# Kernel optimization log

Measured on AMD Instinct MI355X. Metric: run time of the kernel, lower is better.

Reference implementation:

```python
import jax, jax.numpy as jnp
import numpy as np
import math

H, P = 8, 4  # n_heads, num_points


def _interp1d(values, idx):
    # values: (B,H,Lk,D); idx: (B,H,Lq,P) float positions in [0, Lk-1]
    B, h, Lk, D = values.shape
    Lq, p = idx.shape[2], idx.shape[3]
    idx0 = jnp.clip(jnp.floor(idx), 0, Lk - 1).astype(jnp.int32)
    idx1 = jnp.clip(idx0 + 1, 0, Lk - 1)
    w1 = (idx - idx0.astype(idx.dtype))[..., None]          # (B,H,Lq,P,1)
    g0 = jnp.take_along_axis(values, idx0.reshape(B, h, Lq * p)[..., None], axis=2)
    g1 = jnp.take_along_axis(values, idx1.reshape(B, h, Lq * p)[..., None], axis=2)
    g0 = g0.reshape(B, h, Lq, p, D)
    g1 = g1.reshape(B, h, Lq, p, D)
    return (1.0 - w1) * g0 + w1 * g1                         # (B,H,Lq,P,D)


def setup_inputs() -> dict:
    key = jax.random.key(0)
    ks = jax.random.split(key, 8)
    B, L, dm = 4, 4096, 512
    s = 0.02
    return {
        'q_in': jax.random.normal(ks[0], (B, L, dm), jnp.float32),
        'kv_in': jax.random.normal(ks[1], (B, L, dm), jnp.float32),
        'Wq': jax.random.normal(ks[2], (dm, dm), jnp.float32) * s,
        'bq': jnp.zeros((dm,), jnp.float32),
        'Wk': jax.random.normal(ks[3], (dm, dm), jnp.float32) * s,
        'bk': jnp.zeros((dm,), jnp.float32),
        'Wv': jax.random.normal(ks[4], (dm, dm), jnp.float32) * s,
        'bv': jnp.zeros((dm,), jnp.float32),
        'Woff': jax.random.normal(ks[5], (H * P, dm), jnp.float32) * s,
        'boff': jnp.zeros((H * P,), jnp.float32),
        'Wa': jax.random.normal(ks[6], (H * P, dm), jnp.float32) * s,
        'ba': jnp.zeros((H * P,), jnp.float32),
        'Wo': jax.random.normal(ks[7], (dm, dm), jnp.float32) * s,
        'bo': jnp.zeros((dm,), jnp.float32),
    }


def reference(q_in, kv_in, Wq, bq, Wk, bk, Wv, bv, Woff, boff, Wa, ba, Wo, bo):
    B, Lq, dm = q_in.shape
    Lk = kv_in.shape[1]
    D = dm // H
    q = (q_in @ Wq.T + bq).reshape(B, Lq, H, D).transpose(0, 2, 1, 3)   # (B,H,Lq,D)
    k = (kv_in @ Wk.T + bk).reshape(B, Lk, H, D).transpose(0, 2, 1, 3)  # (B,H,Lk,D)
    v = (kv_in @ Wv.T + bv).reshape(B, Lk, H, D).transpose(0, 2, 1, 3)
    offsets = (q_in @ Woff.T + boff).reshape(B, Lq, H, P).transpose(0, 2, 1, 3)  # (B,H,Lq,P)
    logits = (q_in @ Wa.T + ba).reshape(B, Lq, H, P).transpose(0, 2, 1, 3)
    if Lq == Lk:
        base = jnp.arange(Lq, dtype=q_in.dtype).reshape(1, 1, Lq, 1)
    else:
        base = jnp.linspace(0.0, Lk - 1, Lq, dtype=q_in.dtype).reshape(1, 1, Lq, 1)
    idx = jnp.clip(base + offsets, 0.0, float(Lk - 1))
    k_s = _interp1d(k, idx)  # (B,H,Lq,P,D)
    v_s = _interp1d(v, idx)
    dot = jnp.einsum('bhld,bhlpd->bhlp', q, k_s) / math.sqrt(D)
    w = jax.nn.softmax(dot + logits, axis=-1)               # (B,H,Lq,P)
    out = jnp.einsum('bhlp,bhlpd->bhld', w, v_s)            # (B,H,Lq,D)
    out = out.transpose(0, 2, 1, 3).reshape(B, Lq, dm)
    return out @ Wo.T + bo
```

## Files before the change

kernel.cpp:

```cpp
#include <hip/hip_runtime.h>
#include <hip/hip_bf16.h>
#include <math.h>

#define NH 8
#define NP 4
#define DD 64
#define DM 512

typedef unsigned short u16;
typedef unsigned int u32;

using frag_ab = __attribute__((ext_vector_type(8))) short;
using f32x4   = __attribute__((ext_vector_type(4))) float;

__device__ __forceinline__ u16 f2b(float f) {
    u32 u = __float_as_uint(f);
    u32 r = (u + 0x7FFFu + ((u >> 16) & 1u)) >> 16;
    return (u16)r;
}
__device__ __forceinline__ u32 pk2(float x, float y) {
    float2 t; t.x = x; t.y = y;
    __hip_bfloat162 h = __float22bfloat162_rn(t);
    return *(u32*)&h;
}

#define GLOBAL_AS __attribute__((address_space(1)))
#define LDS_AS    __attribute__((address_space(3)))
__device__ __forceinline__ void async_copy16(void* lds, const void* g) {
    __builtin_amdgcn_global_load_lds((const GLOBAL_AS u32*)g, (LDS_AS u32*)lds, 16, 0, 0);
}

#define VMW4_BARRIER() do {                                   \
    asm volatile("s_waitcnt vmcnt(4)" ::: "memory");          \
    __builtin_amdgcn_s_barrier();                             \
    __builtin_amdgcn_sched_barrier(0); } while (0)
#define VMW2_BARRIER() do {                                   \
    asm volatile("s_waitcnt vmcnt(2)" ::: "memory");          \
    __builtin_amdgcn_s_barrier();                             \
    __builtin_amdgcn_sched_barrier(0); } while (0)
#define VMW0_BARRIER() do {                                   \
    asm volatile("s_waitcnt vmcnt(0)" ::: "memory");          \
    __builtin_amdgcn_s_barrier();                             \
    __builtin_amdgcn_sched_barrier(0); } while (0)

__device__ __forceinline__ void compute_phase(
    const u16* __restrict__ sa, const u16* __restrict__ sb,
    int wrow, int wcol, int lr, int kgs, f32x4 (&acc)[4][4])
{
    frag_ab af[4], bfr[4];
#pragma unroll
    for (int i = 0; i < 4; ++i)
        af[i] = *(const frag_ab*)&sa[(wrow + i * 16 + lr) * 32 + kgs];
#pragma unroll
    for (int j = 0; j < 4; ++j)
        bfr[j] = *(const frag_ab*)&sb[(wcol + j * 16 + lr) * 32 + kgs];
    asm volatile("s_waitcnt lgkmcnt(0)" ::: "memory");
    __builtin_amdgcn_s_barrier();
    __builtin_amdgcn_sched_barrier(0);
#pragma unroll
    for (int i = 0; i < 4; ++i)
#pragma unroll
        for (int j = 0; j < 4; ++j)
            acc[i][j] = __builtin_amdgcn_mfma_f32_16x16x32_bf16(
                af[i], bfr[j], acc[i][j], 0, 0, 0);
}

__global__ __launch_bounds__(256) void proj_gemm(
    const u16* __restrict__ q_bf, const u16* __restrict__ kv_bf,
    const u16* __restrict__ Wcat1, const u16* __restrict__ Wcat2,
    const float* __restrict__ bcat1, const float* __restrict__ bcat2,
    u16* __restrict__ q_ws, float* __restrict__ offlog,
    u16* __restrict__ kv_ws)
{
    constexpr int BM = 128, BK = 32;
    __shared__ u16 sA0[BM * BK], sA1[BM * BK];
    __shared__ u16 sB0[BM * BK], sB1[BM * BK];

    const int tid  = threadIdx.x;
    const int wave = tid >> 6;
    const int lane = tid & 63;
    const int m0 = blockIdx.x * BM;
    const bool is_q = blockIdx.y < 5;
    const int n0 = (is_q ? blockIdx.y : blockIdx.y - 5) * BM;
    const int Ncur = is_q ? 576 : 1024;
    const u16* __restrict__ A    = is_q ? q_bf : kv_bf;
    const u16* __restrict__ Wt   = is_q ? Wcat1 : Wcat2;
    const float* __restrict__ bias = is_q ? bcat1 : bcat2;

    const int wrow = 64 * (wave >> 1);
    const int wcol = 64 * (wave & 1);

    f32x4 acc[4][4] = {};
    const int lr = lane & 15;
    const int kg = lane >> 4;
    const int kgs = ((kg ^ ((lr >> 1) & 3)) << 3);
    const int sgo = (((lane & 3) ^ ((lane >> 3) & 3)) << 3);

    float bv4[4];
#pragma unroll
    for (int j = 0; j < 4; ++j)
        bv4[j] = bias[n0 + wcol + j * 16 + lr];

    const int cA = wave * 64 + lane;
    const size_t arow0 = (size_t)(m0 + (cA >> 2)) * DM + sgo;
    const int cA2 = (4 + wave) * 64 + lane;
    const size_t arow1 = (size_t)(m0 + (cA2 >> 2)) * DM + sgo;
    const size_t brow0 = (size_t)(n0 + (cA >> 2)) * DM + sgo;
    const size_t brow1 = (size_t)(n0 + (cA2 >> 2)) * DM + sgo;
    const int ldsA0 = wave * 512, ldsA1 = (4 + wave) * 512;

    auto stage = [&](u16* sa, u16* sb, int k0) {
        async_copy16(&sa[ldsA0], A + arow0 + k0);
        async_copy16(&sa[ldsA1], A + arow1 + k0);
        async_copy16(&sb[ldsA0], Wt + brow0 + k0);
        async_copy16(&sb[ldsA1], Wt + brow1 + k0);
    };

    stage(sA0, sB0, 0);

    for (int ktt = 0; ktt < 8; ++ktt) {
        stage(sA1, sB1, (2 * ktt + 1) << 5);
        VMW4_BARRIER();
        compute_phase(sA0, sB0, wrow, wcol, lr, kgs, acc);
        if (ktt < 7) {
            stage(sA0, sB0, (2 * ktt + 2) << 5);
            VMW4_BARRIER();
        } else {
            VMW0_BARRIER();
        }
        compute_phase(sA1, sB1, wrow, wcol, lr, kgs, acc);
    }

    const int crow0 = (lane >> 4) * 4;
#pragma unroll
    for (int i = 0; i < 4; ++i) {
#pragma unroll
        for (int j = 0; j < 4; ++j) {
            const int colbase = n0 + wcol + j * 16;
            if (colbase >= Ncur) continue;
            const int col = colbase + lr;
            const float bv = bv4[j];
#pragma unroll
            for (int r = 0; r < 4; ++r) {
                const int row = m0 + wrow + i * 16 + crow0 + r;
                const float val = acc[i][j][r] + bv;
                if (!is_q)
                    kv_ws[(size_t)row * 1024 + col] = f2b(val);
                else if (colbase < 512)
                    q_ws[(size_t)row * 512 + col] = f2b(val);
                else
                    offlog[(size_t)row * 64 + (col - 512)] = val;
            }
        }
    }
}

__device__ __forceinline__ void compute_phase8(
    const u16* __restrict__ sa, const u16* __restrict__ sb,
    int wrow, int wcol, int lr, int kgs, f32x4 (&acc)[4][2])
{
    frag_ab af[4], bfr[2];
#pragma unroll
    for (int i = 0; i < 4; ++i)
        af[i] = *(const frag_ab*)&sa[(wrow + i * 16 + lr) * 32 + kgs];
#pragma unroll
    for (int j = 0; j < 2; ++j)
        bfr[j] = *(const frag_ab*)&sb[(wcol + j * 16 + lr) * 32 + kgs];
    asm volatile("s_waitcnt lgkmcnt(0)" ::: "memory");
    __builtin_amdgcn_s_barrier();
    __builtin_amdgcn_sched_barrier(0);
#pragma unroll
    for (int i = 0; i < 4; ++i)
#pragma unroll
        for (int j = 0; j < 2; ++j)
            acc[i][j] = __builtin_amdgcn_mfma_f32_16x16x32_bf16(
                af[i], bfr[j], acc[i][j], 0, 0, 0);
}

__global__ __launch_bounds__(512) void out_gemm(
    const u16* __restrict__ A, const u16* __restrict__ Wt,
    const float* __restrict__ bias, float* __restrict__ C)
{
    constexpr int BM = 128, BK = 32;
    __shared__ u16 sA0[BM * BK], sA1[BM * BK];
    __shared__ u16 sB0[BM * BK], sB1[BM * BK];

    const int tid  = threadIdx.x;
    const int wave = tid >> 6;
    const int lane = tid & 63;
    const int m0 = blockIdx.x * BM;
    const int n0 = blockIdx.y * BM;

    const int wrow = 64 * (wave >> 2);
    const int wcol = 32 * (wave & 3);

    f32x4 acc[4][2] = {};
    const int lr = lane & 15;
    const int kg = lane >> 4;
    const int kgs = ((kg ^ ((lr >> 1) & 3)) << 3);
    const int sgo = (((tid & 3) ^ ((tid >> 3) & 3)) << 3);

    float bv2[2];
#pragma unroll
    for (int j = 0; j < 2; ++j)
        bv2[j] = bias[n0 + wcol + j * 16 + lr];

    const size_t arow = (size_t)(m0 + (tid >> 2)) * DM + sgo;
    const size_t brow = (size_t)(n0 + (tid >> 2)) * DM + sgo;
    const int ldsoff = tid * 8;

    auto stage = [&](u16* sa, u16* sb, int k0) {
        async_copy16(&sa[ldsoff], A + arow + k0);
        async_copy16(&sb[ldsoff], Wt + brow + k0);
    };

    stage(sA0, sB0, 0);

    for (int ktt = 0; ktt < 8; ++ktt) {
        stage(sA1, sB1, (2 * ktt + 1) << 5);
        VMW2_BARRIER();
        compute_phase8(sA0, sB0, wrow, wcol, lr, kgs, acc);
        if (ktt < 7) {
            stage(sA0, sB0, (2 * ktt + 2) << 5);
            VMW2_BARRIER();
        } else {
            VMW0_BARRIER();
        }
        compute_phase8(sA1, sB1, wrow, wcol, lr, kgs, acc);
    }

    const int crow0 = kg * 4;
#pragma unroll
    for (int i = 0; i < 4; ++i) {
#pragma unroll
        for (int j = 0; j < 2; ++j) {
            const int col = n0 + wcol + j * 16 + lr;
            const float bv = bv2[j];
#pragma unroll
            for (int r = 0; r < 4; ++r) {
                const int row = m0 + wrow + i * 16 + crow0 + r;
                C[(size_t)row * 512 + col] = acc[i][j][r] + bv;
            }
        }
    }
}

__global__ __launch_bounds__(256) void prep_weights(
    const float* __restrict__ Wq, const float* __restrict__ Woff,
    const float* __restrict__ Wa, const float* __restrict__ Wk,
    const float* __restrict__ Wv, const float* __restrict__ Wo,
    const float* __restrict__ bq, const float* __restrict__ boff,
    const float* __restrict__ ba, const float* __restrict__ bk,
    const float* __restrict__ bv,
    const float* __restrict__ q_in, const float* __restrict__ kv_in,
    u16* __restrict__ Wcat1, u16* __restrict__ Wcat2, u16* __restrict__ Wob,
    float* __restrict__ bcat1, float* __restrict__ bcat2,
    u16* __restrict__ q_bf, u16* __restrict__ kv_bf, int n8)
{
    const int W4  = 65536;
    const int W4s = 4096;
    const int WEND = 4 * W4 + 2 * W4s;
    const int BEND = WEND + 2048;
    int tid = blockIdx.x * 256 + threadIdx.x;
    if (tid < WEND) {
        const float* src; u16* dst; int off;
        int t = tid;
        if (t < W4)                    { src = Wq;    dst = Wcat1;           off = t; }
        else if ((t -= W4) < W4s)      { src = Woff;  dst = Wcat1 + 262144;  off = t; }
        else if ((t -= W4s) < W4s)     { src = Wa;    dst = Wcat1 + 278528;  off = t; }
        else if ((t -= W4s) < W4)      { src = Wk;    dst = Wcat2;           off = t; }
        else if ((t -= W4) < W4)       { src = Wv;    dst = Wcat2 + 262144;  off = t; }
        else                           { src = Wo;    dst = Wob;             off = t - W4; }
        float4 v = ((const float4*)src)[off];
        ushort4 o;
        o.x = f2b(v.x); o.y = f2b(v.y); o.z = f2b(v.z); o.w = f2b(v.w);
        ((ushort4*)dst)[off] = o;
    } else if (tid < BEND) {
        int j = tid - WEND;
        if (j < 576) {
            bcat1[j] = (j < 512) ? bq[j] : (j < 544 ? boff[j - 512] : ba[j - 544]);
        } else if (j < 1600) {
            int j2 = j - 576;
            bcat2[j2] = (j2 < 512) ? bk[j2] : bv[j2 - 512];
        }
    } else {
        int t = tid - BEND;
        if (t < 2 * n8) {
            const float* src; u16* dst; int off;
            if (t < n8) { src = q_in;  dst = q_bf;  off = t; }
            else        { src = kv_in; dst = kv_bf; off = t - n8; }
            float4 a = ((const float4*)src)[off * 2];
            float4 b = ((const float4*)src)[off * 2 + 1];
            uint4 w;
            w.x = pk2(a.x, a.y); w.y = pk2(a.z, a.w);
            w.z = pk2(b.x, b.y); w.w = pk2(b.z, b.w);
            ((uint4*)dst)[off] = w;
        }
    }
}

#define WAVE_SYNC() do {                                      \
    asm volatile("s_waitcnt lgkmcnt(0)" ::: "memory");        \
    __builtin_amdgcn_sched_barrier(0); } while (0)

__global__ __launch_bounds__(256) void deform_attn_band(
    const u16* __restrict__ q, const u16* __restrict__ kv,
    const float* __restrict__ offlog, u16* __restrict__ out, int B, int L)
{
    __shared__ u16  sVt[4][64 * 40];
    __shared__ float sS[4][16 * 36];
    __shared__ float sW[4][16 * 36];

    const int wave = threadIdx.x >> 6;
    const int lane = threadIdx.x & 63;
    const int gw = blockIdx.x * 4 + wave;
    const int nlb = L >> 4;
    const int lblk = gw % nlb;
    const int bh = gw / nlb;
    const int h = bh % NH;
    const int b = bh / NH;
    const int l0 = lblk << 4;

    u16*  __restrict__ vt = sVt[wave];
    float* __restrict__ Ss = sS[wave];
    float* __restrict__ Ws = sW[wave];

    const size_t brow = (size_t)b * L;
    const int headoff = h * DD;

    const int l_loc = lane >> 2, p = lane & 3;
    const size_t obase = (brow + l0 + l_loc) * 64 + h * 4 + p;
    const float offv  = offlog[obase];
    const float logit = offlog[obase + 32];

    const int fr = lane & 15, kg = lane >> 4;

    const u16* qrow = q + (brow + l0 + fr) * DM + headoff;
    frag_ab qf0 = *(const frag_ab*)(qrow + kg * 8);
    frag_ab qf1 = *(const frag_ab*)(qrow + kg * 8 + 32);

    frag_ab kf[2][2];
#pragma unroll
    for (int jf = 0; jf < 2; ++jf) {
        int rr = l0 - 8 + jf * 16 + fr;
        rr = min(max(rr, 0), L - 1);
        const u16* krow = kv + (brow + rr) * 1024 + headoff;
        kf[jf][0] = *(const frag_ab*)(krow + kg * 8);
        kf[jf][1] = *(const frag_ab*)(krow + kg * 8 + 32);
    }

    const int vr = lane & 31, vd0 = (lane >> 5) * 32;
    int vrr = min(max(l0 - 8 + vr, 0), L - 1);
    const u16* vrow = kv + (brow + vrr) * 1024 + 512 + headoff + vd0;
    frag_ab vl[4];
#pragma unroll
    for (int i = 0; i < 4; ++i)
        vl[i] = *(const frag_ab*)(vrow + i * 8);

    f32x4 accS[2] = {};
#pragma unroll
    for (int jf = 0; jf < 2; ++jf) {
        accS[jf] = __builtin_amdgcn_mfma_f32_16x16x32_bf16(qf0, kf[jf][0], accS[jf], 0, 0, 0);
        accS[jf] = __builtin_amdgcn_mfma_f32_16x16x32_bf16(qf1, kf[jf][1], accS[jf], 0, 0, 0);
    }

#pragma unroll
    for (int i = 0; i < 4; ++i)
#pragma unroll
        for (int j = 0; j < 8; ++j)
            vt[(vd0 + i * 8 + j) * 40 + vr] = (u16)vl[i][j];

#pragma unroll
    for (int jf = 0; jf < 2; ++jf)
#pragma unroll
        for (int r = 0; r < 4; ++r)
            Ss[(kg * 4 + r) * 36 + jf * 16 + fr] = accS[jf][r];

#pragma unroll
    for (int i = 0; i < 9; ++i)
        Ws[lane + 64 * i] = 0.f;

    WAVE_SYNC();

    float pos = fminf(fmaxf((float)(l0 + l_loc) + offv, 0.f), (float)(L - 1));
    float ff = floorf(pos);
    int i0 = (int)ff;
    float fw = pos - ff;
    int c0 = i0 - (l0 - 8);
    c0 = min(max(c0, 0), 30);
    float S0 = Ss[l_loc * 36 + c0];
    float S1 = Ss[l_loc * 36 + c0 + 1];
    float t = (S0 + fw * (S1 - S0)) * 0.125f + logit;
    float m1 = fmaxf(t, __shfl_xor(t, 1));
    float mx = fmaxf(m1, __shfl_xor(m1, 2));
    float e = __expf(t - mx);
    float s1 = e + __shfl_xor(e, 1);
    float ssum = s1 + __shfl_xor(s1, 2);
    float wgt = e * __builtin_amdgcn_rcpf(ssum);
    atomicAdd(&Ws[l_loc * 36 + c0], (1.f - fw) * wgt);
    atomicAdd(&Ws[l_loc * 36 + c0 + 1], fw * wgt);

    WAVE_SYNC();

    float4 w0 = *(const float4*)&Ws[fr * 36 + kg * 8];
    float4 w1 = *(const float4*)&Ws[fr * 36 + kg * 8 + 4];
    frag_ab wf;
    wf[0] = (short)f2b(w0.x); wf[1] = (short)f2b(w0.y);
    wf[2] = (short)f2b(w0.z); wf[3] = (short)f2b(w0.w);
    wf[4] = (short)f2b(w1.x); wf[5] = (short)f2b(w1.y);
    wf[6] = (short)f2b(w1.z); wf[7] = (short)f2b(w1.w);

#pragma unroll
    for (int md = 0; md < 4; ++md) {
        frag_ab af = *(const frag_ab*)&vt[(md * 16 + fr) * 40 + kg * 8];
        f32x4 o = {};
        o = __builtin_amdgcn_mfma_f32_16x16x32_bf16(af, wf, o, 0, 0, 0);
        ushort4 pk;
        pk.x = f2b(o[0]); pk.y = f2b(o[1]); pk.z = f2b(o[2]); pk.w = f2b(o[3]);
        *(ushort4*)&out[(brow + l0 + fr) * DM + headoff + md * 16 + kg * 4] = pk;
    }
}

extern "C" void kernel_launch(void* const* d_in, const int* in_sizes, int n_in,
                              void* d_out, int out_size, void* d_ws, size_t ws_size,
                              hipStream_t stream) {
    const float* q_in  = (const float*)d_in[0];
    const float* kv_in = (const float*)d_in[1];
    const float* Wq = (const float*)d_in[2];  const float* bq = (const float*)d_in[3];
    const float* Wk = (const float*)d_in[4];  const float* bk = (const float*)d_in[5];
    const float* Wv = (const float*)d_in[6];  const float* bv = (const float*)d_in[7];
    const float* Woff=(const float*)d_in[8];  const float* boff=(const float*)d_in[9];
    const float* Wa = (const float*)d_in[10]; const float* ba = (const float*)d_in[11];
    const float* Wo = (const float*)d_in[12]; const float* bo = (const float*)d_in[13];

    const int M = in_sizes[0] / DM;
    const int L = 4096;
    const int B = M / L;

    char* p = (char*)d_ws;
    u16* attn_o = (u16*)p;               p += (size_t)M * DM * 2;
    u16* Wcat1  = (u16*)p;               p += (size_t)768 * DM * 2;
    u16* Wcat2  = (u16*)p;               p += (size_t)1024 * DM * 2;
    u16* Wob    = (u16*)p;               p += (size_t)DM * DM * 2;
    float* bcat1= (float*)p;             p += 640 * 4;
    float* bcat2= (float*)p;             p += 1024 * 4;
    u16* q_ws   = (u16*)p;               p += (size_t)M * DM * 2;
    u16* kv_ws  = (u16*)p;               p += (size_t)M * 1024 * 2;
    float* offlog = (float*)p;           p += (size_t)M * 64 * 4;

    u16* q_bf  = attn_o;
    u16* kv_bf = (u16*)d_out;

    const int n8 = M * DM / 8;
    const int prep_threads = 4 * 65536 + 2 * 4096 + 2048 + 2 * n8;
    hipLaunchKernelGGL(prep_weights, dim3((prep_threads + 255) / 256), dim3(256), 0, stream,
                       Wq, Woff, Wa, Wk, Wv, Wo, bq, boff, ba, bk, bv,
                       q_in, kv_in,
                       Wcat1, Wcat2, Wob, bcat1, bcat2, q_bf, kv_bf, n8);

    hipLaunchKernelGGL(proj_gemm, dim3(M / 128, 13), dim3(256), 0, stream,
                       q_bf, kv_bf, Wcat1, Wcat2, bcat1, bcat2,
                       q_ws, offlog, kv_ws);

    int nwaves = B * NH * (L / 16);
    hipLaunchKernelGGL(deform_attn_band, dim3(nwaves / 4), dim3(256), 0, stream,
                       q_ws, kv_ws, offlog, attn_o, B, L);

    hipLaunchKernelGGL(out_gemm, dim3(M / 128, 4), dim3(512), 0, stream,
                       attn_o, Wob, bo, (float*)d_out);
}
```

Before: 202.3 us.

## Deepen projection GEMM pipeline to four LDS stages and alias score/weight buffers

The projection GEMM moves from a double-buffered to a four-stage LDS ring. Loads are issued two tiles ahead, and the extra barrier inside compute_phase is removed, so each k-step has one wait and one barrier instead of two. This aims to hide global-load latency better, at the cost of twice the LDS for that kernel, which may reduce occupancy. In the attention kernel, the score and weight scratch buffers now share one LDS array, with an extra wave sync before the weights are zeroed, to cut LDS usage.

```diff
diff --git a/kernel.cpp b/kernel.cpp
--- a/kernel.cpp
+++ b/kernel.cpp
@@ -30,19 +30,6 @@
     __builtin_amdgcn_global_load_lds((const GLOBAL_AS u32*)g, (LDS_AS u32*)lds, 16, 0, 0);
 }
 
-#define VMW4_BARRIER() do {                                   \
-    asm volatile("s_waitcnt vmcnt(4)" ::: "memory");          \
-    __builtin_amdgcn_s_barrier();                             \
-    __builtin_amdgcn_sched_barrier(0); } while (0)
-#define VMW2_BARRIER() do {                                   \
-    asm volatile("s_waitcnt vmcnt(2)" ::: "memory");          \
-    __builtin_amdgcn_s_barrier();                             \
-    __builtin_amdgcn_sched_barrier(0); } while (0)
-#define VMW0_BARRIER() do {                                   \
-    asm volatile("s_waitcnt vmcnt(0)" ::: "memory");          \
-    __builtin_amdgcn_s_barrier();                             \
-    __builtin_amdgcn_sched_barrier(0); } while (0)
-
 __device__ __forceinline__ void compute_phase(
     const u16* __restrict__ sa, const u16* __restrict__ sb,
     int wrow, int wcol, int lr, int kgs, f32x4 (&acc)[4][4])
@@ -55,7 +42,6 @@
     for (int j = 0; j < 4; ++j)
         bfr[j] = *(const frag_ab*)&sb[(wcol + j * 16 + lr) * 32 + kgs];
     asm volatile("s_waitcnt lgkmcnt(0)" ::: "memory");
-    __builtin_amdgcn_s_barrier();
     __builtin_amdgcn_sched_barrier(0);
 #pragma unroll
     for (int i = 0; i < 4; ++i)
@@ -64,6 +50,14 @@
             acc[i][j] = __builtin_amdgcn_mfma_f32_16x16x32_bf16(
                 af[i], bfr[j], acc[i][j], 0, 0, 0);
 }
+
+#define PROJ_PHASE(SAR, SBR, VMN)                               \
+    do {                                                        \
+        asm volatile("s_waitcnt vmcnt(" VMN ")" ::: "memory");  \
+        __builtin_amdgcn_s_barrier();                           \
+        __builtin_amdgcn_sched_barrier(0);                      \
+        compute_phase(SAR, SBR, wrow, wcol, lr, kgs, acc);      \
+    } while (0)
 
 __global__ __launch_bounds__(256) void proj_gemm(
     const u16* __restrict__ q_bf, const u16* __restrict__ kv_bf,
@@ -73,8 +67,8 @@
     u16* __restrict__ kv_ws)
 {
     constexpr int BM = 128, BK = 32;
-    __shared__ u16 sA0[BM * BK], sA1[BM * BK];
-    __shared__ u16 sB0[BM * BK], sB1[BM * BK];
+    __shared__ u16 sA0[BM * BK], sA1[BM * BK], sA2[BM * BK], sA3[BM * BK];
+    __shared__ u16 sB0[BM * BK], sB1[BM * BK], sB2[BM * BK], sB3[BM * BK];
 
     const int tid  = threadIdx.x;
     const int wave = tid >> 6;
@@ -117,19 +111,19 @@
     };
 
     stage(sA0, sB0, 0);
-
-    for (int ktt = 0; ktt < 8; ++ktt) {
-        stage(sA1, sB1, (2 * ktt + 1) << 5);
-        VMW4_BARRIER();
-        compute_phase(sA0, sB0, wrow, wcol, lr, kgs, acc);
-        if (ktt < 7) {
-            stage(sA0, sB0, (2 * ktt + 2) << 5);
-            VMW4_BARRIER();
-        } else {
-            VMW0_BARRIER();
-        }
-        compute_phase(sA1, sB1, wrow, wcol, lr, kgs, acc);
-    }
+    stage(sA1, sB1, 32);
+
+    for (int k = 0; k < 3; ++k) {
+        const int t0k = k << 7;
+        stage(sA2, sB2, t0k + 64);  PROJ_PHASE(sA0, sB0, "8");
+        stage(sA3, sB3, t0k + 96);  PROJ_PHASE(sA1, sB1, "8");
+        stage(sA0, sB0, t0k + 128); PROJ_PHASE(sA2, sB2, "8");
+        stage(sA1, sB1, t0k + 160); PROJ_PHASE(sA3, sB3, "8");
+    }
+    stage(sA2, sB2, 448); PROJ_PHASE(sA0, sB0, "8");
+    stage(sA3, sB3, 480); PROJ_PHASE(sA1, sB1, "8");
+    PROJ_PHASE(sA2, sB2, "4");
+    PROJ_PHASE(sA3, sB3, "0");
 
     const int crow0 = (lane >> 4) * 4;
 #pragma unroll
@@ -154,6 +148,15 @@
         }
     }
 }
+
+#define VMW2_BARRIER() do {                                   \
+    asm volatile("s_waitcnt vmcnt(2)" ::: "memory");          \
+    __builtin_amdgcn_s_barrier();                             \
+    __builtin_amdgcn_sched_barrier(0); } while (0)
+#define VMW0_BARRIER() do {                                   \
+    asm volatile("s_waitcnt vmcnt(0)" ::: "memory");          \
+    __builtin_amdgcn_s_barrier();                             \
+    __builtin_amdgcn_sched_barrier(0); } while (0)
 
 __device__ __forceinline__ void compute_phase8(
     const u16* __restrict__ sa, const u16* __restrict__ sb,
@@ -308,8 +311,7 @@
     const float* __restrict__ offlog, u16* __restrict__ out, int B, int L)
 {
     __shared__ u16  sVt[4][64 * 40];
-    __shared__ float sS[4][16 * 36];
-    __shared__ float sW[4][16 * 36];
+    __shared__ float sSW[4][16 * 36];
 
     const int wave = threadIdx.x >> 6;
     const int lane = threadIdx.x & 63;
@@ -322,8 +324,8 @@
     const int l0 = lblk << 4;
 
     u16*  __restrict__ vt = sVt[wave];
-    float* __restrict__ Ss = sS[wave];
-    float* __restrict__ Ws = sW[wave];
+    float* __restrict__ Ss = sSW[wave];
+    float* __restrict__ Ws = sSW[wave];
 
     const size_t brow = (size_t)b * L;
     const int headoff = h * DD;
@@ -375,10 +377,6 @@
 #pragma unroll
         for (int r = 0; r < 4; ++r)
             Ss[(kg * 4 + r) * 36 + jf * 16 + fr] = accS[jf][r];
-
-#pragma unroll
-    for (int i = 0; i < 9; ++i)
-        Ws[lane + 64 * i] = 0.f;
 
     WAVE_SYNC();
 
@@ -390,6 +388,8 @@
     c0 = min(max(c0, 0), 30);
     float S0 = Ss[l_loc * 36 + c0];
     float S1 = Ss[l_loc * 36 + c0 + 1];
+    WAVE_SYNC();
+
     float t = (S0 + fw * (S1 - S0)) * 0.125f + logit;
     float m1 = fmaxf(t, __shfl_xor(t, 1));
     float mx = fmaxf(m1, __shfl_xor(m1, 2));
@@ -397,9 +397,13 @@
     float s1 = e + __shfl_xor(e, 1);
     float ssum = s1 + __shfl_xor(s1, 2);
     float wgt = e * __builtin_amdgcn_rcpf(ssum);
+
+#pragma unroll
+    for (int i = 0; i < 9; ++i)
+        Ws[lane + 64 * i] = 0.f;
+    WAVE_SYNC();
     atomicAdd(&Ws[l_loc * 36 + c0], (1.f - fw) * wgt);
     atomicAdd(&Ws[l_loc * 36 + c0 + 1], fw * wgt);
-
     WAVE_SYNC();
 
     float4 w0 = *(const float4*)&Ws[fr * 36 + kg * 8];
```

After: 210.1 us. 1.04x slower.

## Load projection B fragments directly from pre-packed global weights into registers

Applied to the files above, without the earlier changes.

The weight-prep kernel now stores the Q/K/V/offset/logit projection weights in a fragment-packed layout, so each lane's MFMA B operand is one contiguous 16-byte chunk. The projection GEMM then loads B fragments straight from global memory into registers with double buffering, which removes the B LDS tiles and their async copies. Only the A tile is still staged through LDS, and the wait count is adjusted for the extra outstanding loads. In exchange it needs more registers and relies on the cache to serve weights that several blocks share.

```diff
diff --git a/kernel.cpp b/kernel.cpp
--- a/kernel.cpp
+++ b/kernel.cpp
@@ -30,8 +30,8 @@
     __builtin_amdgcn_global_load_lds((const GLOBAL_AS u32*)g, (LDS_AS u32*)lds, 16, 0, 0);
 }
 
-#define VMW4_BARRIER() do {                                   \
-    asm volatile("s_waitcnt vmcnt(4)" ::: "memory");          \
+#define VMW6_BARRIER() do {                                   \
+    asm volatile("s_waitcnt vmcnt(6)" ::: "memory");          \
     __builtin_amdgcn_s_barrier();                             \
     __builtin_amdgcn_sched_barrier(0); } while (0)
 #define VMW2_BARRIER() do {                                   \
@@ -43,17 +43,14 @@
     __builtin_amdgcn_s_barrier();                             \
     __builtin_amdgcn_sched_barrier(0); } while (0)
 
-__device__ __forceinline__ void compute_phase(
-    const u16* __restrict__ sa, const u16* __restrict__ sb,
-    int wrow, int wcol, int lr, int kgs, f32x4 (&acc)[4][4])
-{
-    frag_ab af[4], bfr[4];
+__device__ __forceinline__ void compute_afb(
+    const u16* __restrict__ sa, int wrow, int lr, int kgs,
+    const frag_ab (&bfr)[4], f32x4 (&acc)[4][4])
+{
+    frag_ab af[4];
 #pragma unroll
     for (int i = 0; i < 4; ++i)
         af[i] = *(const frag_ab*)&sa[(wrow + i * 16 + lr) * 32 + kgs];
-#pragma unroll
-    for (int j = 0; j < 4; ++j)
-        bfr[j] = *(const frag_ab*)&sb[(wcol + j * 16 + lr) * 32 + kgs];
     asm volatile("s_waitcnt lgkmcnt(0)" ::: "memory");
     __builtin_amdgcn_s_barrier();
     __builtin_amdgcn_sched_barrier(0);
@@ -74,7 +71,6 @@
 {
     constexpr int BM = 128, BK = 32;
     __shared__ u16 sA0[BM * BK], sA1[BM * BK];
-    __shared__ u16 sB0[BM * BK], sB1[BM * BK];
 
     const int tid  = threadIdx.x;
     const int wave = tid >> 6;
@@ -105,30 +101,37 @@
     const size_t arow0 = (size_t)(m0 + (cA >> 2)) * DM + sgo;
     const int cA2 = (4 + wave) * 64 + lane;
     const size_t arow1 = (size_t)(m0 + (cA2 >> 2)) * DM + sgo;
-    const size_t brow0 = (size_t)(n0 + (cA >> 2)) * DM + sgo;
-    const size_t brow1 = (size_t)(n0 + (cA2 >> 2)) * DM + sgo;
     const int ldsA0 = wave * 512, ldsA1 = (4 + wave) * 512;
 
-    auto stage = [&](u16* sa, u16* sb, int k0) {
+    const size_t bfr_base = (size_t)((n0 + wcol) >> 4) * 16 * 512 + (size_t)lane * 8;
+
+    auto stageA = [&](u16* sa, int k0) {
         async_copy16(&sa[ldsA0], A + arow0 + k0);
         async_copy16(&sa[ldsA1], A + arow1 + k0);
-        async_copy16(&sb[ldsA0], Wt + brow0 + k0);
-        async_copy16(&sb[ldsA1], Wt + brow1 + k0);
     };
-
-    stage(sA0, sB0, 0);
+    auto loadB = [&](frag_ab (&b)[4], int kt) {
+#pragma unroll
+        for (int j = 0; j < 4; ++j)
+            b[j] = *(const frag_ab*)(Wt + bfr_base + (size_t)(j * 16 + kt) * 512);
+    };
+
+    frag_ab b0[4], b1[4];
+    stageA(sA0, 0);
+    loadB(b0, 0);
 
     for (int ktt = 0; ktt < 8; ++ktt) {
-        stage(sA1, sB1, (2 * ktt + 1) << 5);
-        VMW4_BARRIER();
-        compute_phase(sA0, sB0, wrow, wcol, lr, kgs, acc);
+        stageA(sA1, (2 * ktt + 1) << 5);
+        loadB(b1, 2 * ktt + 1);
+        VMW6_BARRIER();
+        compute_afb(sA0, wrow, lr, kgs, b0, acc);
         if (ktt < 7) {
-            stage(sA0, sB0, (2 * ktt + 2) << 5);
-            VMW4_BARRIER();
+            stageA(sA0, (2 * ktt + 2) << 5);
+            loadB(b0, 2 * ktt + 2);
+            VMW6_BARRIER();
         } else {
             VMW0_BARRIER();
         }
-        compute_phase(sA1, sB1, wrow, wcol, lr, kgs, acc);
+        compute_afb(sA1, wrow, lr, kgs, b1, acc);
     }
 
     const int crow0 = (lane >> 4) * 4;
@@ -263,18 +266,25 @@
     const int BEND = WEND + 2048;
     int tid = blockIdx.x * 256 + threadIdx.x;
     if (tid < WEND) {
-        const float* src; u16* dst; int off;
-        int t = tid;
-        if (t < W4)                    { src = Wq;    dst = Wcat1;           off = t; }
-        else if ((t -= W4) < W4s)      { src = Woff;  dst = Wcat1 + 262144;  off = t; }
-        else if ((t -= W4s) < W4s)     { src = Wa;    dst = Wcat1 + 278528;  off = t; }
-        else if ((t -= W4s) < W4)      { src = Wk;    dst = Wcat2;           off = t; }
-        else if ((t -= W4) < W4)       { src = Wv;    dst = Wcat2 + 262144;  off = t; }
-        else                           { src = Wo;    dst = Wob;             off = t - W4; }
+        const float* src; u16* dst; int t = tid; int off; int lin; bool packed = true;
+        if (t < W4)                    { src = Wq;   dst = Wcat1; off = t;      lin = off * 4; }
+        else if ((t -= W4) < W4s)      { src = Woff; dst = Wcat1; off = t;      lin = 262144 + off * 4; }
+        else if ((t -= W4s) < W4s)     { src = Wa;   dst = Wcat1; off = t;      lin = 278528 + off * 4; }
+        else if ((t -= W4s) < W4)      { src = Wk;   dst = Wcat2; off = t;      lin = off * 4; }
+        else if ((t -= W4) < W4)       { src = Wv;   dst = Wcat2; off = t;      lin = 262144 + off * 4; }
+        else                           { src = Wo;   dst = Wob;   off = t - W4; lin = off * 4; packed = false; }
         float4 v = ((const float4*)src)[off];
         ushort4 o;
         o.x = f2b(v.x); o.y = f2b(v.y); o.z = f2b(v.z); o.w = f2b(v.w);
-        ((ushort4*)dst)[off] = o;
+        if (!packed) {
+            ((ushort4*)dst)[lin >> 2] = o;
+        } else {
+            const int n = lin >> 9, k = lin & 511;
+            const int nb = n >> 4, lr = n & 15;
+            const int kt = k >> 5, kg = (k >> 3) & 3, e0 = k & 7;
+            const int elem = ((nb * 16 + kt) << 9) + ((kg * 16 + lr) << 3) + e0;
+            *(ushort4*)&dst[elem] = o;
+        }
     } else if (tid < BEND) {
         int j = tid - WEND;
         if (j < 576) {
```

Result: no change. 201.7 us (-0.3%).
